# Performance work log

Hardware: AMD Instinct MI355X
Metric: run time of the kernel (lower is better)

## Reference

```python
import jax, jax.numpy as jnp
import numpy as np

B, S, DIN, DOUT = 2, 2048, 4096, 4096


def setup_inputs() -> dict:
    key = jax.random.key(0)
    k1, k2 = jax.random.split(key)
    x = jax.random.normal(k1, (B, S, DIN), dtype=jnp.float32)
    weight = jax.random.normal(k2, (DOUT, DIN), dtype=jnp.float32) * 0.02
    # xnor init for row scaling pattern
    mean = weight.mean(-1, keepdims=True)                      # [DOUT,1]
    scale = jnp.abs(weight - mean).mean(-1, keepdims=True)     # [DOUT,1]
    wscale = scale
    wbias = mean
    return {"x": x, "weight": weight, "wscale": wscale, "wbias": wbias}


def reference(x, weight, wscale, wbias):
    # STE binarization: forward = sign(weight) (grad handled in bwd module)
    w_bin = jnp.sign(weight)
    w = wscale * w_bin + wbias                                 # [DOUT, DIN]
    # F.linear(x, w): x @ w.T, no bias
    out = jnp.einsum('bsk,nk->bsn', x, w)
    return out
```

## Files before the change

### kernel.cpp

```cpp
#include <hip/hip_runtime.h>
#include <stdint.h>


#define MDIM 4096
#define NDIM 4096
#define KDIM 4096

typedef int int4v  __attribute__((ext_vector_type(4)));
typedef int int16v __attribute__((ext_vector_type(16)));

__device__ __forceinline__ int pack4_rn(float a, float b, float c, float d, float inv) {
  int ia = __float2int_rn(a * inv) & 0xff;
  int ib = __float2int_rn(b * inv) & 0xff;
  int ic = __float2int_rn(c * inv) & 0xff;
  int id = __float2int_rn(d * inv) & 0xff;
  return ia | (ib << 8) | (ic << 16) | (id << 24);
}

__device__ __forceinline__ int sgn8(float v) {
  return (v > 0.f) ? 1 : ((v < 0.f) ? 0xff : 0);
}

__global__ __launch_bounds__(256) void prep_kernel(
    const float* __restrict__ x, const float* __restrict__ w,
    char* __restrict__ xq, char* __restrict__ wsg,
    float* __restrict__ xscale, float* __restrict__ sumx) {
  const int b = blockIdx.x;
  const int tid = threadIdx.x;
  if (b < MDIM) {
    const int row = b;
    const float4* xr = (const float4*)(x + (size_t)row * KDIM);
    float4 v[4];
    float s = 0.f, amax = 0.f;
#pragma unroll
    for (int u = 0; u < 4; ++u) {
      v[u] = xr[u * 256 + tid];
      s += v[u].x + v[u].y + v[u].z + v[u].w;
      amax = fmaxf(amax, fmaxf(fmaxf(fabsf(v[u].x), fabsf(v[u].y)),
                               fmaxf(fabsf(v[u].z), fabsf(v[u].w))));
    }
#pragma unroll
    for (int off = 32; off > 0; off >>= 1) {
      s += __shfl_down(s, off, 64);
      amax = fmaxf(amax, __shfl_down(amax, off, 64));
    }
    __shared__ float rs[4], rm[4], bcast;
    if ((tid & 63) == 0) { rs[tid >> 6] = s; rm[tid >> 6] = amax; }
    __syncthreads();
    if (tid == 0) {
      sumx[row] = rs[0] + rs[1] + rs[2] + rs[3];
      float mt = fmaxf(fmaxf(rm[0], rm[1]), fmaxf(rm[2], rm[3]));
      xscale[row] = mt * (1.f / 127.f);
      bcast = (mt > 0.f) ? 127.f / mt : 0.f;
    }
    __syncthreads();
    const float inv = bcast;
    int* xo = (int*)(xq + (size_t)row * KDIM);
#pragma unroll
    for (int u = 0; u < 4; ++u)
      xo[u * 256 + tid] = pack4_rn(v[u].x, v[u].y, v[u].z, v[u].w, inv);
  } else {
    const size_t base = (size_t)(b - MDIM) * (256 * 4);
    const float4* wr = (const float4*)w;
    int* wo = (int*)wsg;
#pragma unroll
    for (int u = 0; u < 4; ++u) {
      size_t i = base + u * 256 + tid;
      float4 v = wr[i];
      wo[i] = sgn8(v.x) | (sgn8(v.y) << 8) | (sgn8(v.z) << 16) | (sgn8(v.w) << 24);
    }
  }
}

__global__ __launch_bounds__(512, 2) void gemm_bin_i8_8phase(
    const char* __restrict__ A, const char* __restrict__ Bs,
    const float* __restrict__ wscale, const float* __restrict__ wbias,
    const float* __restrict__ xscale, const float* __restrict__ sumx,
    float* __restrict__ C) {
  __shared__ __align__(16) char sm[131072];

  const int bm = blockIdx.x >> 4, bn = blockIdx.x & 15;
  const int tm0 = bm * 256, tn0 = bn * 256;
  const int tid = threadIdx.x;
  const int lane = tid & 63, wave = tid >> 6;
  const int col32 = lane & 31, hl = lane >> 5;
  const int wr = wave >> 2, wc = wave & 3;

  int16v acc[4][2];
#pragma unroll
  for (int mi = 0; mi < 4; ++mi)
#pragma unroll
    for (int nj = 0; nj < 2; ++nj)
#pragma unroll
      for (int r = 0; r < 16; ++r) acc[mi][nj][r] = 0;

  int aOff[2][4], bOff[2][2];
#pragma unroll
  for (int ks2 = 0; ks2 < 2; ++ks2) {
#pragma unroll
    for (int mi = 0; mi < 4; ++mi) {
      int row = wr * 128 + mi * 32 + col32;
      int sw = (row >> 1) & 3;
      aOff[ks2][mi] = row * 64 + (((ks2 * 2 + hl) ^ sw) & 3) * 16;
    }
#pragma unroll
    for (int nj = 0; nj < 2; ++nj) {
      int row = wc * 64 + nj * 32 + col32;
      int sw = (row >> 1) & 3;
      bOff[ks2][nj] = 65536 + row * 64 + (((ks2 * 2 + hl) ^ sw) & 3) * 16;
    }
  }

  const int u0 = tid, u1 = tid + 512;
  const int r0 = u0 >> 2, r1 = u1 >> 2;
  const int c0 = (u0 & 3) ^ ((r0 >> 1) & 3);
  const int c1 = (u1 & 3) ^ ((r1 >> 1) & 3);
  const char* gA0 = A + (size_t)(tm0 + r0) * KDIM + c0 * 16;
  const char* gA1 = A + (size_t)(tm0 + r1) * KDIM + c1 * 16;
  const char* gB0 = Bs + (size_t)(tn0 + r0) * KDIM + c0 * 16;
  const char* gB1 = Bs + (size_t)(tn0 + r1) * KDIM + c1 * 16;
  const int ldsu0 = tid * 16, ldsu1 = 8192 + tid * 16;

#define STAGE_A(BUF, KH, KOFS)                                                    \
  do {                                                                            \
    const int base_ = ((BUF) * 2 + (KH)) * 16384;                                 \
    __builtin_amdgcn_global_load_lds(                                             \
        (const __attribute__((address_space(1))) void*)(gA0 + (KOFS)),            \
        (__attribute__((address_space(3))) void*)(sm + base_ + ldsu0), 16, 0, 0); \
    __builtin_amdgcn_global_load_lds(                                             \
        (const __attribute__((address_space(1))) void*)(gA1 + (KOFS)),            \
        (__attribute__((address_space(3))) void*)(sm + base_ + ldsu1), 16, 0, 0); \
  } while (0)

#define STAGE_B(BUF, KH, KOFS)                                                    \
  do {                                                                            \
    const int base_ = 65536 + ((BUF) * 2 + (KH)) * 16384;                         \
    __builtin_amdgcn_global_load_lds(                                             \
        (const __attribute__((address_space(1))) void*)(gB0 + (KOFS)),            \
        (__attribute__((address_space(3))) void*)(sm + base_ + ldsu0), 16, 0, 0); \
    __builtin_amdgcn_global_load_lds(                                             \
        (const __attribute__((address_space(1))) void*)(gB1 + (KOFS)),            \
        (__attribute__((address_space(3))) void*)(sm + base_ + ldsu1), 16, 0, 0); \
  } while (0)

#define BAR __builtin_amdgcn_s_barrier()
#define CK4 asm volatile("s_waitcnt vmcnt(4)\n\ts_barrier" ::: "memory")
#define CK0 asm volatile("s_waitcnt vmcnt(0)\n\ts_barrier" ::: "memory")

#define PHASE(BUF, KS, KS2, CKBAR, ...)                                           \
  do {                                                                            \
    int4v af[4], bq[2];                                                           \
    _Pragma("unroll") for (int mi_ = 0; mi_ < 4; ++mi_)                           \
        af[mi_] = *(const int4v*)(sm + ((BUF) * 2 + (KS)) * 16384 + aOff[KS2][mi_]); \
    _Pragma("unroll") for (int nj_ = 0; nj_ < 2; ++nj_)                           \
        bq[nj_] = *(const int4v*)(sm + ((BUF) * 2 + (KS)) * 16384 + bOff[KS2][nj_]); \
    __VA_ARGS__;                                                                  \
    __builtin_amdgcn_s_barrier();                                                 \
    asm volatile("s_waitcnt lgkmcnt(0)" ::: "memory");                            \
    __builtin_amdgcn_sched_barrier(0);                                            \
    __builtin_amdgcn_s_setprio(1);                                                \
    _Pragma("unroll") for (int mi_ = 0; mi_ < 4; ++mi_)                           \
        _Pragma("unroll") for (int nj_ = 0; nj_ < 2; ++nj_)                       \
            acc[mi_][nj_] = __builtin_amdgcn_mfma_i32_32x32x32_i8(                \
                af[mi_], bq[nj_], acc[mi_][nj_], 0, 0, 0);                        \
    __builtin_amdgcn_s_setprio(0);                                                \
    CKBAR;                                                                        \
  } while (0)

#define ITER_FULL(BUF, TAU)                                                       \
  do {                                                                            \
    PHASE(BUF, 0, 0, BAR, STAGE_A((BUF) ^ 1, 1, ((TAU) + 1) * 128 + 64));         \
    PHASE(BUF, 0, 1, BAR, STAGE_B((BUF) ^ 1, 1, ((TAU) + 1) * 128 + 64));         \
    PHASE(BUF, 1, 0, BAR, STAGE_A(BUF, 0, ((TAU) + 2) * 128));                    \
    PHASE(BUF, 1, 1, CK4, STAGE_B(BUF, 0, ((TAU) + 2) * 128));                    \
  } while (0)

  STAGE_A(0, 0, 0);
  STAGE_B(0, 0, 0);
  STAGE_A(0, 1, 64);
  STAGE_B(0, 1, 64);
  STAGE_A(1, 0, 128);
  STAGE_B(1, 0, 128);
  CK4;

#pragma unroll 1
  for (int t = 0; t < 30; t += 2) {
    ITER_FULL(0, t);
    ITER_FULL(1, t + 1);
  }
  PHASE(0, 0, 0, BAR, STAGE_A(1, 1, 31 * 128 + 64));
  PHASE(0, 0, 1, BAR, STAGE_B(1, 1, 31 * 128 + 64));
  PHASE(0, 1, 0, BAR, (void)0);
  PHASE(0, 1, 1, CK0, (void)0);
  PHASE(1, 0, 0, BAR, (void)0);
  PHASE(1, 0, 1, BAR, (void)0);
  PHASE(1, 1, 0, BAR, (void)0);
  PHASE(1, 1, 1, BAR, (void)0);

#undef ITER_FULL
#undef PHASE
#undef BAR
#undef CK4
#undef CK0
#undef STAGE_A
#undef STAGE_B

  float wsv[2], wbv[2];
#pragma unroll
  for (int nj = 0; nj < 2; ++nj) {
    int n = tn0 + wc * 64 + nj * 32 + col32;
    wsv[nj] = wscale[n];
    wbv[nj] = wbias[n];
  }
#pragma unroll
  for (int mi = 0; mi < 4; ++mi) {
#pragma unroll
    for (int reg = 0; reg < 16; ++reg) {
      int m = tm0 + wr * 128 + mi * 32 + (reg & 3) + 8 * (reg >> 2) + 4 * hl;
      float xs = xscale[m];
      float sx = sumx[m];
      float* crow = C + (size_t)m * NDIM + tn0 + wc * 64 + col32;
#pragma unroll
      for (int nj = 0; nj < 2; ++nj)
        crow[nj * 32] = wsv[nj] * xs * (float)acc[mi][nj][reg] + wbv[nj] * sx;
    }
  }
}

extern "C" void kernel_launch(void* const* d_in, const int* in_sizes, int n_in,
                              void* d_out, int out_size, void* d_ws, size_t ws_size,
                              hipStream_t stream) {
  const float* x      = (const float*)d_in[0];
  const float* weight = (const float*)d_in[1];
  const float* wscale = (const float*)d_in[2];
  const float* wbias  = (const float*)d_in[3];
  float* out = (float*)d_out;

  char* xq  = (char*)d_ws;
  char* wsg = xq + (size_t)MDIM * KDIM;
  float* xscale = (float*)(wsg + (size_t)NDIM * KDIM);
  float* sumx   = xscale + MDIM;

  prep_kernel<<<MDIM + (NDIM * KDIM) / (16 * 256), 256, 0, stream>>>(
      x, weight, xq, wsg, xscale, sumx);
  gemm_bin_i8_8phase<<<(MDIM / 256) * (NDIM / 256), 512, 0, stream>>>(
      xq, wsg, wscale, wbias, xscale, sumx, out);
}
```

Before: 236.7 us.

## Double-buffer LDS fragment reads in registers to overlap with MFMA

```diff
diff --git a/kernel.cpp b/kernel.cpp
--- a/kernel.cpp
+++ b/kernel.cpp
@@ -72,7 +72,7 @@
   }
 }
 
-__global__ __launch_bounds__(512, 2) void gemm_bin_i8_8phase(
+__global__ __launch_bounds__(512, 2) void gemm_bin_i8_pipe(
     const char* __restrict__ A, const char* __restrict__ Bs,
     const float* __restrict__ wscale, const float* __restrict__ wbias,
     const float* __restrict__ xscale, const float* __restrict__ sumx,
@@ -93,6 +93,8 @@
     for (int nj = 0; nj < 2; ++nj)
 #pragma unroll
       for (int r = 0; r < 16; ++r) acc[mi][nj][r] = 0;
+
+  int4v afA[4], bqA[2], afB[4], bqB[2];
 
   int aOff[2][4], bOff[2][2];
 #pragma unroll
@@ -143,36 +145,57 @@
         (__attribute__((address_space(3))) void*)(sm + base_ + ldsu1), 16, 0, 0); \
   } while (0)
 
-#define BAR __builtin_amdgcn_s_barrier()
-#define CK4 asm volatile("s_waitcnt vmcnt(4)\n\ts_barrier" ::: "memory")
-#define CK0 asm volatile("s_waitcnt vmcnt(0)\n\ts_barrier" ::: "memory")
-
-#define PHASE(BUF, KS, KS2, CKBAR, ...)                                           \
-  do {                                                                            \
-    int4v af[4], bq[2];                                                           \
+#define DSRD(SET, BUF, KS, KS2)                                                   \
+  do {                                                                            \
     _Pragma("unroll") for (int mi_ = 0; mi_ < 4; ++mi_)                           \
-        af[mi_] = *(const int4v*)(sm + ((BUF) * 2 + (KS)) * 16384 + aOff[KS2][mi_]); \
+        af##SET[mi_] =                                                            \
+            *(const int4v*)(sm + ((BUF) * 2 + (KS)) * 16384 + aOff[KS2][mi_]);    \
     _Pragma("unroll") for (int nj_ = 0; nj_ < 2; ++nj_)                           \
-        bq[nj_] = *(const int4v*)(sm + ((BUF) * 2 + (KS)) * 16384 + bOff[KS2][nj_]); \
-    __VA_ARGS__;                                                                  \
-    __builtin_amdgcn_s_barrier();                                                 \
-    asm volatile("s_waitcnt lgkmcnt(0)" ::: "memory");                            \
-    __builtin_amdgcn_sched_barrier(0);                                            \
+        bq##SET[nj_] =                                                            \
+            *(const int4v*)(sm + ((BUF) * 2 + (KS)) * 16384 + bOff[KS2][nj_]);    \
+  } while (0)
+
+#define MFMA8(SET)                                                                \
+  do {                                                                            \
     __builtin_amdgcn_s_setprio(1);                                                \
     _Pragma("unroll") for (int mi_ = 0; mi_ < 4; ++mi_)                           \
         _Pragma("unroll") for (int nj_ = 0; nj_ < 2; ++nj_)                       \
             acc[mi_][nj_] = __builtin_amdgcn_mfma_i32_32x32x32_i8(                \
-                af[mi_], bq[nj_], acc[mi_][nj_], 0, 0, 0);                        \
+                af##SET[mi_], bq##SET[nj_], acc[mi_][nj_], 0, 0, 0);              \
     __builtin_amdgcn_s_setprio(0);                                                \
-    CKBAR;                                                                        \
-  } while (0)
-
-#define ITER_FULL(BUF, TAU)                                                       \
-  do {                                                                            \
-    PHASE(BUF, 0, 0, BAR, STAGE_A((BUF) ^ 1, 1, ((TAU) + 1) * 128 + 64));         \
-    PHASE(BUF, 0, 1, BAR, STAGE_B((BUF) ^ 1, 1, ((TAU) + 1) * 128 + 64));         \
-    PHASE(BUF, 1, 0, BAR, STAGE_A(BUF, 0, ((TAU) + 2) * 128));                    \
-    PHASE(BUF, 1, 1, CK4, STAGE_B(BUF, 0, ((TAU) + 2) * 128));                    \
+  } while (0)
+
+#define WAITL6                                                                    \
+  do {                                                                            \
+    asm volatile("s_waitcnt lgkmcnt(6)" ::: "memory");                            \
+    __builtin_amdgcn_sched_barrier(0);                                            \
+  } while (0)
+#define WAITL0                                                                    \
+  do {                                                                            \
+    asm volatile("s_waitcnt lgkmcnt(0)" ::: "memory");                            \
+    __builtin_amdgcn_sched_barrier(0);                                            \
+  } while (0)
+
+#define BARO __builtin_amdgcn_s_barrier()
+#define CK6  asm volatile("s_waitcnt vmcnt(6)\n\ts_barrier" ::: "memory")
+#define CK4  asm volatile("s_waitcnt vmcnt(4)\n\ts_barrier" ::: "memory")
+#define CK0  asm volatile("s_waitcnt vmcnt(0)\n\ts_barrier" ::: "memory")
+
+#define PHASEP(CSET, NSET, NBUF, NKS, NKS2, STAGEOP, ENDSYNC)                     \
+  do {                                                                            \
+    DSRD(NSET, NBUF, NKS, NKS2);                                                  \
+    STAGEOP;                                                                      \
+    WAITL6;                                                                       \
+    MFMA8(CSET);                                                                  \
+    ENDSYNC;                                                                      \
+  } while (0)
+
+#define TILE_MAIN(BUF, TAU)                                                       \
+  do {                                                                            \
+    PHASEP(A, B, BUF, 0, 1, STAGE_A((BUF) ^ 1, 1, ((TAU) + 1) * 128 + 64), BARO); \
+    PHASEP(B, A, BUF, 1, 0, STAGE_B((BUF) ^ 1, 1, ((TAU) + 1) * 128 + 64), BARO); \
+    PHASEP(A, B, BUF, 1, 1, STAGE_A(BUF, 0, ((TAU) + 2) * 128), CK6);             \
+    PHASEP(B, A, (BUF) ^ 1, 0, 0, STAGE_B(BUF, 0, ((TAU) + 2) * 128), CK4);       \
   } while (0)
 
   STAGE_A(0, 0, 0);
@@ -182,26 +205,34 @@
   STAGE_A(1, 0, 128);
   STAGE_B(1, 0, 128);
   CK4;
+  DSRD(A, 0, 0, 0);
 
 #pragma unroll 1
   for (int t = 0; t < 30; t += 2) {
-    ITER_FULL(0, t);
-    ITER_FULL(1, t + 1);
-  }
-  PHASE(0, 0, 0, BAR, STAGE_A(1, 1, 31 * 128 + 64));
-  PHASE(0, 0, 1, BAR, STAGE_B(1, 1, 31 * 128 + 64));
-  PHASE(0, 1, 0, BAR, (void)0);
-  PHASE(0, 1, 1, CK0, (void)0);
-  PHASE(1, 0, 0, BAR, (void)0);
-  PHASE(1, 0, 1, BAR, (void)0);
-  PHASE(1, 1, 0, BAR, (void)0);
-  PHASE(1, 1, 1, BAR, (void)0);
-
-#undef ITER_FULL
-#undef PHASE
-#undef BAR
+    TILE_MAIN(0, t);
+    TILE_MAIN(1, t + 1);
+  }
+
+  PHASEP(A, B, 0, 0, 1, STAGE_A(1, 1, 31 * 128 + 64), BARO);
+  PHASEP(B, A, 0, 1, 0, STAGE_B(1, 1, 31 * 128 + 64), BARO);
+  PHASEP(A, B, 0, 1, 1, (void)0, CK4);
+  PHASEP(B, A, 1, 0, 0, (void)0, CK0);
+  PHASEP(A, B, 1, 0, 1, (void)0, BARO);
+  PHASEP(B, A, 1, 1, 0, (void)0, BARO);
+  PHASEP(A, B, 1, 1, 1, (void)0, BARO);
+  WAITL0;
+  MFMA8(B);
+
+#undef TILE_MAIN
+#undef PHASEP
+#undef BARO
+#undef CK6
 #undef CK4
 #undef CK0
+#undef WAITL6
+#undef WAITL0
+#undef MFMA8
+#undef DSRD
 #undef STAGE_A
 #undef STAGE_B
 
@@ -243,6 +274,6 @@
 
   prep_kernel<<<MDIM + (NDIM * KDIM) / (16 * 256), 256, 0, stream>>>(
       x, weight, xq, wsg, xscale, sumx);
-  gemm_bin_i8_8phase<<<(MDIM / 256) * (NDIM / 256), 512, 0, stream>>>(
+  gemm_bin_i8_pipe<<<(MDIM / 256) * (NDIM / 256), 512, 0, stream>>>(
       xq, wsg, wscale, wbias, xscale, sumx, out);
 }
```

After: 234.1 us. About the same (-1.1%).
